# Kernel tuning notes

Hardware: AMD Instinct MI355X
Metric: run time of the kernel (lower is better)

## Reference

```python
import jax, jax.numpy as jnp
import numpy as np

T, D_IN, D_OUT, E, K = 4096, 1024, 1024, 8, 2
H = max(D_IN, D_OUT) * 4  # 4096, per nbHidden = max(nbIn, nbOut) * 4


def setup_inputs() -> dict:
    key = jax.random.key(0)
    ks = jax.random.split(key, 12)
    s = 0.02
    return {
        "x": jax.random.normal(ks[0], (T, D_IN), dtype=jnp.float32),
        "noise": jax.random.normal(ks[1], (T, E), dtype=jnp.float32),
        "gate_w": jax.random.normal(ks[2], (D_IN, E), dtype=jnp.float32) * s,
        "gate_b": jnp.zeros((E,), dtype=jnp.float32),
        "noise_w": jax.random.normal(ks[3], (D_IN, E), dtype=jnp.float32) * s,
        "noise_b": jnp.zeros((E,), dtype=jnp.float32),
        "w1": jax.random.normal(ks[4], (E, D_IN, H), dtype=jnp.float32) * s,
        "b1": jnp.zeros((E, H), dtype=jnp.float32),
        "w2": jax.random.normal(ks[5], (E, H, D_OUT), dtype=jnp.float32) * s,
        "b2": jnp.zeros((E, D_OUT), dtype=jnp.float32),
    }


def reference(x, noise, gate_w, gate_b, noise_w, noise_b, w1, b1, w2, b2):
    # Noisy gating: gate(x) + randn * softplus(noise(x))
    logits = (x @ gate_w + gate_b) + noise * jax.nn.softplus(x @ noise_w + noise_b)  # [T, E]
    topk_vals, topk_idx = jax.lax.top_k(logits, K)          # [T, K]
    gate_prob = jax.nn.softmax(topk_vals, axis=1)           # softmax over selected K logits
    rows = jnp.arange(x.shape[0])[:, None]
    weights = jnp.zeros((x.shape[0], E), dtype=x.dtype).at[rows, topk_idx].set(gate_prob)  # [T, E]

    # Dense path (memMode=False): run every expert MLP on all tokens, masked combine.
    h = jax.nn.relu(jnp.einsum("ti,eih->teh", x, w1) + b1[None])   # [T, E, H]
    expert_out = jnp.einsum("teh,eho->teo", h, w2) + b2[None]       # [T, E, O]
    x_out = jnp.einsum("te,teo->to", weights, expert_out)           # [T, O]
    return x_out, weights
```

## Files before the change

### kernel.cpp

```cpp
#include <hip/hip_runtime.h>

#define T_TOK 4096
#define DIN   1024
#define DOUT  1024
#define NEXP  8
#define HDIM  4096
#define RCAP  9216
#define MT128 80

typedef float f32x4 __attribute__((ext_vector_type(4)));
typedef short bf16x8 __attribute__((ext_vector_type(8)));
typedef unsigned short u16x4 __attribute__((ext_vector_type(4)));
typedef unsigned short u16x8 __attribute__((ext_vector_type(8)));

__device__ __forceinline__ float bf2f(unsigned short u) {
    union { unsigned int i; float f; } v; v.i = ((unsigned int)u) << 16; return v.f;
}
__device__ __forceinline__ unsigned short f2bf(float f) {
    union { unsigned int i; float f; } v; v.f = f;
    unsigned int r = v.i + 0x7FFFu + ((v.i >> 16) & 1u);
    return (unsigned short)(r >> 16);
}

__global__ __launch_bounds__(64) void gating_kernel(
    const float* __restrict__ x, const float* __restrict__ noise,
    const float* __restrict__ gw, const float* __restrict__ gb,
    const float* __restrict__ nw, const float* __restrict__ nb,
    float* __restrict__ wout,
    int* __restrict__ tok_e, float* __restrict__ tok_p)
{
    int t = blockIdx.x;
    int lane = threadIdx.x;
    const float* xr = x + (size_t)t * DIN;
    double ag[NEXP], an[NEXP];
#pragma unroll
    for (int e = 0; e < NEXP; ++e) { ag[e] = 0.0; an[e] = 0.0; }
    for (int d = lane; d < DIN; d += 64) {
        double xv = (double)xr[d];
        const f32x4* g4 = (const f32x4*)(gw + (size_t)d * NEXP);
        const f32x4* n4 = (const f32x4*)(nw + (size_t)d * NEXP);
        f32x4 ga = g4[0], gbv = g4[1], na = n4[0], nbv = n4[1];
#pragma unroll
        for (int j = 0; j < 4; ++j) {
            ag[j]     += xv * (double)ga[j];
            ag[4 + j] += xv * (double)gbv[j];
            an[j]     += xv * (double)na[j];
            an[4 + j] += xv * (double)nbv[j];
        }
    }
#pragma unroll
    for (int e = 0; e < NEXP; ++e) {
        double g = ag[e], n = an[e];
#pragma unroll
        for (int m = 32; m > 0; m >>= 1) { g += __shfl_xor(g, m); n += __shfl_xor(n, m); }
        ag[e] = g; an[e] = n;
    }
    double lg[NEXP];
#pragma unroll
    for (int e = 0; e < NEXP; ++e) {
        double z = an[e] + (double)nb[e];
        double sp = fmax(z, 0.0) + log1p(exp(-fabs(z)));
        lg[e] = ag[e] + (double)gb[e] + (double)noise[(size_t)t * NEXP + e] * sp;
    }
    int i0 = 0; double v0 = lg[0];
#pragma unroll
    for (int e = 1; e < NEXP; ++e) if (lg[e] > v0) { v0 = lg[e]; i0 = e; }
    int i1 = -1; double v1 = -1.0e300;
#pragma unroll
    for (int e = 0; e < NEXP; ++e) if (e != i0 && lg[e] > v1) { v1 = lg[e]; i1 = e; }
    double d1 = exp(v1 - v0);
    float p0 = (float)(1.0 / (1.0 + d1));
    float p1 = (float)(d1 / (1.0 + d1));
    if (lane < NEXP) {
        float wv = (lane == i0) ? p0 : ((lane == i1) ? p1 : 0.0f);
        wout[(size_t)t * NEXP + lane] = wv;
    }
    if (lane == 0) {
        tok_e[2 * t] = i0;     tok_e[2 * t + 1] = i1;
        tok_p[2 * t] = p0;     tok_p[2 * t + 1] = p1;
    }
}

__global__ __launch_bounds__(256) void scan_kernel(
    const int* __restrict__ tok_e, int* __restrict__ tok_slot, int* __restrict__ cnt)
{
    __shared__ int wsum[4];
    int e = blockIdx.x;
    int tid = threadIdx.x;
    int wv = tid >> 6;
    int lane = tid & 63;
    int base = 0;
    for (int c = 0; c < 2 * T_TOK; c += 256) {
        int i = c + tid;
        int m = (tok_e[i] == e) ? 1 : 0;
        unsigned long long bal = __ballot(m);
        int before = __popcll(bal & ((1ull << lane) - 1ull));
        if (lane == 0) wsum[wv] = __popcll(bal);
        __syncthreads();
        int woff = 0;
#pragma unroll
        for (int w = 0; w < 4; ++w) if (w < wv) woff += wsum[w];
        if (m) tok_slot[i] = base + woff + before;
        int tot = wsum[0] + wsum[1] + wsum[2] + wsum[3];
        __syncthreads();
        base += tot;
    }
    if (tid == 0) cnt[e] = base;
}

__global__ void prefix_kernel(const int* __restrict__ cnt, int* __restrict__ poff,
                              int* __restrict__ t2e, int* __restrict__ trow)
{
    if (threadIdx.x != 0 || blockIdx.x != 0) return;
    int base = 0, a = 0;
    for (int e = 0; e < NEXP; ++e) {
        poff[e] = base;
        int c = cnt[e];
        int nt = (c + 127) >> 7;
        for (int i = 0; i < nt; ++i) { t2e[a] = e; trow[a] = base + (i << 7); ++a; }
        base += nt << 7;
    }
    for (; a < MT128; ++a) { t2e[a] = -1; trow[a] = 0; }
}

__global__ __launch_bounds__(256) void gather_kernel(
    const float* __restrict__ x, const int* __restrict__ tok_e,
    const int* __restrict__ tok_slot, const int* __restrict__ poff,
    unsigned short* __restrict__ Xg)
{
    int b = blockIdx.x;
    int t = b >> 1, k = b & 1;
    int e = tok_e[2 * t + k];
    int row = poff[e] + tok_slot[2 * t + k];
    int c = threadIdx.x << 2;
    f32x4 v = *(const f32x4*)(x + (size_t)t * DIN + c);
    u16x4 o;
#pragma unroll
    for (int j = 0; j < 4; ++j) o[j] = f2bf(v[j]);
    *(u16x4*)(Xg + (size_t)row * DIN + c) = o;
}

__global__ __launch_bounds__(256) void convw_kernel(
    const float* __restrict__ W, unsigned short* __restrict__ Wt, int K, int N)
{
    __shared__ float tile[64][65];
    int e = blockIdx.x;
    int k0 = blockIdx.y << 6;
    int n0 = blockIdx.z << 6;
    int tid = threadIdx.x;
    const float* src = W + ((size_t)e * K + k0) * N + n0;
    int r = tid >> 4, c4 = (tid & 15) << 2;
#pragma unroll
    for (int i = 0; i < 4; ++i) {
        f32x4 v = *(const f32x4*)(src + (size_t)(r + (i << 4)) * N + c4);
        *(f32x4*)(&tile[r + (i << 4)][c4]) = v;
    }
    __syncthreads();
    unsigned short* dst = Wt + ((size_t)e * N + n0) * K + k0;
#pragma unroll
    for (int i = 0; i < 2; ++i) {
        int u = (i << 8) + tid;
        int n = u >> 3, kk = (u & 7) << 3;
        u16x8 o;
#pragma unroll
        for (int q = 0; q < 8; ++q) o[q] = f2bf(tile[kk + q][n]);
        *(u16x8*)(dst + (size_t)n * K + kk) = o;
    }
}

__global__ __launch_bounds__(256, 4) void gemm64_kernel(
    const unsigned short* __restrict__ A, int lda,
    const unsigned short* __restrict__ Bt, int ldb, int N, int KLEN,
    unsigned short* __restrict__ C,
    const float* __restrict__ bias,
    const int* __restrict__ t2e, const int* __restrict__ trow,
    int nbshift, int relu)
{
    int nwg = gridDim.x;
    int cpx = nwg >> 3;
    int wg = ((blockIdx.x & 7) * cpx) + (blockIdx.x >> 3);
    int tileid = wg >> nbshift;
    int nb = wg & ((1 << nbshift) - 1);

    int e = t2e[tileid];
    if (e < 0) return;
    int row0 = trow[tileid];
    int n0 = nb << 7;

    __shared__ __align__(16) unsigned short As[128 * 64];
    __shared__ __align__(16) unsigned short Bs[128 * 64];

    int tid = threadIdx.x;
    int lane = tid & 63;
    int wv = tid >> 6;
    int wr = (wv >> 1) << 6;
    int wc = (wv & 1) << 6;

    const unsigned short* Ab = A + (size_t)row0 * lda;
    const unsigned short* Bb = Bt + ((size_t)e * N + n0) * ldb;

    f32x4 acc[4][4] = {};

    int sr_lo = tid >> 3;
    int sp = tid & 7;
    int hr = lane & 15;
    int q4 = lane >> 4;

    int nkt = KLEN >> 6;
    for (int kt = 0; kt < nkt; ++kt) {
        __syncthreads();
        int kb = kt << 6;
#pragma unroll
        for (int i = 0; i < 4; ++i) {
            int r = (i << 5) + sr_lo;
            int col = ((sp ^ (r & 7)) << 3);
            int u = (i << 8) + tid;
            __builtin_amdgcn_global_load_lds(
                (const __attribute__((address_space(1))) void*)(Ab + (size_t)r * lda + kb + col),
                (__attribute__((address_space(3))) void*)(&As[u << 3]), 16, 0, 0);
            __builtin_amdgcn_global_load_lds(
                (const __attribute__((address_space(1))) void*)(Bb + (size_t)r * ldb + kb + col),
                (__attribute__((address_space(3))) void*)(&Bs[u << 3]), 16, 0, 0);
        }
        __syncthreads();
#pragma unroll
        for (int kq = 0; kq < 2; ++kq) {
            int slog = (kq << 2) | q4;
            bf16x8 af[4], bfv[4];
#pragma unroll
            for (int m = 0; m < 4; ++m) {
                int r = wr + (m << 4) + hr;
                af[m] = *(const bf16x8*)(&As[(r << 6) + ((slog ^ (r & 7)) << 3)]);
            }
#pragma unroll
            for (int n = 0; n < 4; ++n) {
                int r = wc + (n << 4) + hr;
                bfv[n] = *(const bf16x8*)(&Bs[(r << 6) + ((slog ^ (r & 7)) << 3)]);
            }
#pragma unroll
            for (int m = 0; m < 4; ++m)
#pragma unroll
                for (int n = 0; n < 4; ++n)
                    acc[m][n] = __builtin_amdgcn_mfma_f32_16x16x32_bf16(af[m], bfv[n], acc[m][n], 0, 0, 0);
        }
    }

    int rq = q4 << 2;
    int cl = hr;
#pragma unroll
    for (int n = 0; n < 4; ++n) {
        int col = wc + (n << 4) + cl;
        float bv = bias[(size_t)e * N + n0 + col];
#pragma unroll
        for (int m = 0; m < 4; ++m) {
#pragma unroll
            for (int r = 0; r < 4; ++r) {
                int row = wr + (m << 4) + rq + r;
                float v = acc[m][n][r] + bv;
                if (relu) v = fmaxf(v, 0.0f);
                C[(size_t)(row0 + row) * N + n0 + col] = f2bf(v);
            }
        }
    }
}

__global__ __launch_bounds__(256) void combine_kernel(
    const unsigned short* __restrict__ O, const int* __restrict__ tok_e,
    const int* __restrict__ tok_slot, const float* __restrict__ tok_p,
    const int* __restrict__ poff, float* __restrict__ xout)
{
    int t = blockIdx.x;
    int e0 = tok_e[2 * t], e1 = tok_e[2 * t + 1];
    int r0 = poff[e0] + tok_slot[2 * t];
    int r1 = poff[e1] + tok_slot[2 * t + 1];
    float p0 = tok_p[2 * t], p1 = tok_p[2 * t + 1];
    int c = threadIdx.x << 2;
    u16x4 a = *(const u16x4*)(O + (size_t)r0 * DOUT + c);
    u16x4 b = *(const u16x4*)(O + (size_t)r1 * DOUT + c);
    f32x4 r;
#pragma unroll
    for (int j = 0; j < 4; ++j) r[j] = p0 * bf2f(a[j]) + p1 * bf2f(b[j]);
    *(f32x4*)(xout + (size_t)t * DOUT + c) = r;
}

extern "C" void kernel_launch(void* const* d_in, const int* in_sizes, int n_in,
                              void* d_out, int out_size, void* d_ws, size_t ws_size,
                              hipStream_t stream)
{
    const float* x     = (const float*)d_in[0];
    const float* noise = (const float*)d_in[1];
    const float* gw    = (const float*)d_in[2];
    const float* gb    = (const float*)d_in[3];
    const float* nw    = (const float*)d_in[4];
    const float* nb    = (const float*)d_in[5];
    const float* w1    = (const float*)d_in[6];
    const float* b1    = (const float*)d_in[7];
    const float* w2    = (const float*)d_in[8];
    const float* b2    = (const float*)d_in[9];
    float* xout = (float*)d_out;
    float* wout = xout + (size_t)T_TOK * DOUT;

    char* ws = (char*)d_ws;
    int*   cnt      = (int*)(ws + 0);
    int*   poff     = (int*)(ws + 256);
    int*   t2e      = (int*)(ws + 512);
    int*   trow     = (int*)(ws + 1024);
    int*   tok_e    = (int*)(ws + 2048);
    int*   tok_slot = (int*)(ws + 34816);
    float* tok_p    = (float*)(ws + 67584);
    size_t oXg = 104448;
    unsigned short* Xg  = (unsigned short*)(ws + oXg);
    unsigned short* O   = Xg;
    size_t oH  = oXg + (size_t)RCAP * DIN * 2;
    unsigned short* H   = (unsigned short*)(ws + oH);
    size_t oW1 = oH + (size_t)RCAP * HDIM * 2;
    unsigned short* W1t = (unsigned short*)(ws + oW1);
    size_t oW2 = oW1 + (size_t)NEXP * HDIM * DIN * 2;
    unsigned short* W2t = (unsigned short*)(ws + oW2);

    gating_kernel<<<T_TOK, 64, 0, stream>>>(x, noise, gw, gb, nw, nb,
                                            wout, tok_e, tok_p);
    scan_kernel<<<NEXP, 256, 0, stream>>>(tok_e, tok_slot, cnt);
    prefix_kernel<<<1, 1, 0, stream>>>(cnt, poff, t2e, trow);
    gather_kernel<<<2 * T_TOK, 256, 0, stream>>>(x, tok_e, tok_slot, poff, Xg);
    convw_kernel<<<dim3(NEXP, DIN / 64, HDIM / 64), 256, 0, stream>>>(w1, W1t, DIN, HDIM);
    convw_kernel<<<dim3(NEXP, HDIM / 64, DOUT / 64), 256, 0, stream>>>(w2, W2t, HDIM, DOUT);
    gemm64_kernel<<<MT128 * 32, 256, 0, stream>>>(
        Xg, DIN, W1t, DIN, HDIM, DIN, H, b1, t2e, trow, 5, 1);
    gemm64_kernel<<<MT128 * 8, 256, 0, stream>>>(
        H, HDIM, W2t, HDIM, DOUT, HDIM, O, b2, t2e, trow, 3, 0);
    combine_kernel<<<T_TOK, 256, 0, stream>>>(O, tok_e, tok_slot, tok_p, poff, xout);
}
```

Before: 356.7 us.

## Double-buffer LDS tiles in expert GEMM to overlap loads with MFMA

Replaces the single LDS tile pair with two ping-pong buffers so the global-to-LDS load of the next K tile is issued while the MFMA work on the current tile runs. This removes the load-then-wait stall at every K step and one barrier per iteration. In exchange, LDS use doubles to 64KB per block and the launch bound drops from 4 to 2 blocks per CU, which reduces occupancy and the latency hiding that came from running more blocks at once. The loop assumes an even number of K tiles.

```diff
diff --git a/kernel.cpp b/kernel.cpp
--- a/kernel.cpp
+++ b/kernel.cpp
@@ -168,7 +168,7 @@
     }
 }
 
-__global__ __launch_bounds__(256, 4) void gemm64_kernel(
+__global__ __launch_bounds__(256, 2) void gemm64_kernel(
     const unsigned short* __restrict__ A, int lda,
     const unsigned short* __restrict__ Bt, int ldb, int N, int KLEN,
     unsigned short* __restrict__ C,
@@ -187,8 +187,10 @@
     int row0 = trow[tileid];
     int n0 = nb << 7;
 
-    __shared__ __align__(16) unsigned short As[128 * 64];
-    __shared__ __align__(16) unsigned short Bs[128 * 64];
+    __shared__ __align__(16) unsigned short As0[128 * 64];
+    __shared__ __align__(16) unsigned short Bs0[128 * 64];
+    __shared__ __align__(16) unsigned short As1[128 * 64];
+    __shared__ __align__(16) unsigned short Bs1[128 * 64];
 
     int tid = threadIdx.x;
     int lane = tid & 63;
@@ -206,44 +208,60 @@
     int hr = lane & 15;
     int q4 = lane >> 4;
 
+#define STAGE(AS, BS, KT)                                                              \
+    {                                                                                  \
+        int kb = (KT) << 6;                                                            \
+        _Pragma("unroll")                                                              \
+        for (int i = 0; i < 4; ++i) {                                                  \
+            int r = (i << 5) + sr_lo;                                                  \
+            int col = ((sp ^ (r & 7)) << 3);                                           \
+            int u = (i << 8) + tid;                                                    \
+            __builtin_amdgcn_global_load_lds(                                          \
+                (const __attribute__((address_space(1))) void*)(Ab + (size_t)r * lda + kb + col), \
+                (__attribute__((address_space(3))) void*)(&AS[u << 3]), 16, 0, 0);     \
+            __builtin_amdgcn_global_load_lds(                                          \
+                (const __attribute__((address_space(1))) void*)(Bb + (size_t)r * ldb + kb + col), \
+                (__attribute__((address_space(3))) void*)(&BS[u << 3]), 16, 0, 0);     \
+        }                                                                              \
+    }
+
+#define COMPUTE(AS, BS)                                                                \
+    {                                                                                  \
+        _Pragma("unroll")                                                              \
+        for (int kq = 0; kq < 2; ++kq) {                                               \
+            int slog = (kq << 2) | q4;                                                 \
+            bf16x8 af[4], bfv[4];                                                      \
+            _Pragma("unroll")                                                          \
+            for (int m = 0; m < 4; ++m) {                                              \
+                int r = wr + (m << 4) + hr;                                            \
+                af[m] = *(const bf16x8*)(&AS[(r << 6) + ((slog ^ (r & 7)) << 3)]);     \
+            }                                                                          \
+            _Pragma("unroll")                                                          \
+            for (int n = 0; n < 4; ++n) {                                              \
+                int r = wc + (n << 4) + hr;                                            \
+                bfv[n] = *(const bf16x8*)(&BS[(r << 6) + ((slog ^ (r & 7)) << 3)]);    \
+            }                                                                          \
+            _Pragma("unroll")                                                          \
+            for (int m = 0; m < 4; ++m)                                                \
+                _Pragma("unroll")                                                      \
+                for (int n = 0; n < 4; ++n)                                            \
+                    acc[m][n] = __builtin_amdgcn_mfma_f32_16x16x32_bf16(af[m], bfv[n], acc[m][n], 0, 0, 0); \
+        }                                                                              \
+    }
+
     int nkt = KLEN >> 6;
-    for (int kt = 0; kt < nkt; ++kt) {
+    STAGE(As0, Bs0, 0);
+    __syncthreads();
+    for (int kt = 0; kt < nkt; kt += 2) {
+        STAGE(As1, Bs1, kt + 1);
+        COMPUTE(As0, Bs0);
         __syncthreads();
-        int kb = kt << 6;
-#pragma unroll
-        for (int i = 0; i < 4; ++i) {
-            int r = (i << 5) + sr_lo;
-            int col = ((sp ^ (r & 7)) << 3);
-            int u = (i << 8) + tid;
-            __builtin_amdgcn_global_load_lds(
-                (const __attribute__((address_space(1))) void*)(Ab + (size_t)r * lda + kb + col),
-                (__attribute__((address_space(3))) void*)(&As[u << 3]), 16, 0, 0);
-            __builtin_amdgcn_global_load_lds(
-                (const __attribute__((address_space(1))) void*)(Bb + (size_t)r * ldb + kb + col),
-                (__attribute__((address_space(3))) void*)(&Bs[u << 3]), 16, 0, 0);
-        }
+        if (kt + 2 < nkt) STAGE(As0, Bs0, kt + 2);
+        COMPUTE(As1, Bs1);
         __syncthreads();
-#pragma unroll
-        for (int kq = 0; kq < 2; ++kq) {
-            int slog = (kq << 2) | q4;
-            bf16x8 af[4], bfv[4];
-#pragma unroll
-            for (int m = 0; m < 4; ++m) {
-                int r = wr + (m << 4) + hr;
-                af[m] = *(const bf16x8*)(&As[(r << 6) + ((slog ^ (r & 7)) << 3)]);
-            }
-#pragma unroll
-            for (int n = 0; n < 4; ++n) {
-                int r = wc + (n << 4) + hr;
-                bfv[n] = *(const bf16x8*)(&Bs[(r << 6) + ((slog ^ (r & 7)) << 3)]);
-            }
-#pragma unroll
-            for (int m = 0; m < 4; ++m)
-#pragma unroll
-                for (int n = 0; n < 4; ++n)
-                    acc[m][n] = __builtin_amdgcn_mfma_f32_16x16x32_bf16(af[m], bfv[n], acc[m][n], 0, 0, 0);
-        }
-    }
+    }
+#undef STAGE
+#undef COMPUTE
 
     int rq = q4 << 2;
     int cl = hr;
```

Measured after the change: 390.5 us. 1.09x slower.

## Use 128x256 tile 512-thread kernel for first expert GEMM and merge weight conversions

Applied to the files above, without the earlier changes.

Replaces the first expert GEMM with a dedicated kernel using 512 threads and a 128x256 output tile, where each wave computes a 64x64 sub-tile from swizzled LDS filled by direct global-to-LDS loads. This raises arithmetic intensity per loaded tile and halves the number of workgroups. The two weight transpose/convert launches are also merged into one kernel to save a launch. The larger tile uses more LDS and registers per block, which may reduce occupancy, and the GEMM loop remains single-buffered.

```diff
diff --git a/kernel.cpp b/kernel.cpp
--- a/kernel.cpp
+++ b/kernel.cpp
@@ -140,13 +140,22 @@
     *(u16x4*)(Xg + (size_t)row * DIN + c) = o;
 }
 
-__global__ __launch_bounds__(256) void convw_kernel(
-    const float* __restrict__ W, unsigned short* __restrict__ Wt, int K, int N)
+__global__ __launch_bounds__(256) void convw2x_kernel(
+    const float* __restrict__ w1, unsigned short* __restrict__ W1t,
+    const float* __restrict__ w2, unsigned short* __restrict__ W2t)
 {
     __shared__ float tile[64][65];
     int e = blockIdx.x;
-    int k0 = blockIdx.y << 6;
-    int n0 = blockIdx.z << 6;
+    int idx = blockIdx.y;
+    const float* W; unsigned short* Wt; int K, N, k0, n0;
+    if (idx < 1024) {
+        W = w1; Wt = W1t; K = DIN; N = HDIM;
+        k0 = (idx >> 6) << 6; n0 = (idx & 63) << 6;
+    } else {
+        int i2 = idx - 1024;
+        W = w2; Wt = W2t; K = HDIM; N = DOUT;
+        k0 = (i2 >> 4) << 6; n0 = (i2 & 15) << 6;
+    }
     int tid = threadIdx.x;
     const float* src = W + ((size_t)e * K + k0) * N + n0;
     int r = tid >> 4, c4 = (tid & 15) << 2;
@@ -165,6 +174,102 @@
 #pragma unroll
         for (int q = 0; q < 8; ++q) o[q] = f2bf(tile[kk + q][n]);
         *(u16x8*)(dst + (size_t)n * K + kk) = o;
+    }
+}
+
+__global__ __launch_bounds__(512, 4) void gemm1_wide_kernel(
+    const unsigned short* __restrict__ A,
+    const unsigned short* __restrict__ Bt,
+    unsigned short* __restrict__ C,
+    const float* __restrict__ bias,
+    const int* __restrict__ t2e, const int* __restrict__ trow)
+{
+    const int lda = DIN, ldb = DIN, N = HDIM;
+    int cpx = gridDim.x >> 3;
+    int wg = ((blockIdx.x & 7) * cpx) + (blockIdx.x >> 3);
+    int tileid = wg >> 4;
+    int nb = wg & 15;
+    int e = t2e[tileid];
+    if (e < 0) return;
+    int row0 = trow[tileid];
+    int n0 = nb << 8;
+
+    __shared__ __align__(16) unsigned short As[128 * 64];
+    __shared__ __align__(16) unsigned short Bs[256 * 64];
+
+    int tid = threadIdx.x;
+    int lane = tid & 63;
+    int wv = tid >> 6;
+    int wr = (wv >> 2) << 6;
+    int wc = (wv & 3) << 6;
+
+    const unsigned short* Ab = A + (size_t)row0 * lda;
+    const unsigned short* Bb = Bt + ((size_t)e * N + n0) * ldb;
+
+    f32x4 acc[4][4] = {};
+    int hr = lane & 15;
+    int q4 = lane >> 4;
+
+    for (int kt = 0; kt < 16; ++kt) {
+        __syncthreads();
+        int kb = kt << 6;
+#pragma unroll
+        for (int i = 0; i < 2; ++i) {
+            int u = (i << 9) + tid;
+            int r = u >> 3, sp = u & 7;
+            int col = ((sp ^ (r & 7)) << 3);
+            __builtin_amdgcn_global_load_lds(
+                (const __attribute__((address_space(1))) void*)(Ab + (size_t)r * lda + kb + col),
+                (__attribute__((address_space(3))) void*)(&As[u << 3]), 16, 0, 0);
+        }
+#pragma unroll
+        for (int i = 0; i < 4; ++i) {
+            int u = (i << 9) + tid;
+            int r = u >> 3, sp = u & 7;
+            int col = ((sp ^ (r & 7)) << 3);
+            __builtin_amdgcn_global_load_lds(
+                (const __attribute__((address_space(1))) void*)(Bb + (size_t)r * ldb + kb + col),
+                (__attribute__((address_space(3))) void*)(&Bs[u << 3]), 16, 0, 0);
+        }
+        __syncthreads();
+#pragma unroll
+        for (int kq = 0; kq < 2; ++kq) {
+            int slog = (kq << 2) | q4;
+            bf16x8 af[4], bfv[4];
+#pragma unroll
+            for (int m = 0; m < 4; ++m) {
+                int r = wr + (m << 4) + hr;
+                af[m] = *(const bf16x8*)(&As[(r << 6) + ((slog ^ (r & 7)) << 3)]);
+            }
+#pragma unroll
+            for (int n = 0; n < 4; ++n) {
+                int r = wc + (n << 4) + hr;
+                bfv[n] = *(const bf16x8*)(&Bs[(r << 6) + ((slog ^ (r & 7)) << 3)]);
+            }
+#pragma unroll
+            for (int m = 0; m < 4; ++m)
+#pragma unroll
+                for (int n = 0; n < 4; ++n)
+                    acc[m][n] = __builtin_amdgcn_mfma_f32_16x16x32_bf16(af[m], bfv[n], acc[m][n], 0, 0, 0);
+        }
+    }
+
+    int rq = q4 << 2;
+    int cl = hr;
+#pragma unroll
+    for (int n = 0; n < 4; ++n) {
+        int col = wc + (n << 4) + cl;
+        float bv = bias[(size_t)e * N + n0 + col];
+#pragma unroll
+        for (int m = 0; m < 4; ++m) {
+#pragma unroll
+            for (int r = 0; r < 4; ++r) {
+                int row = wr + (m << 4) + rq + r;
+                float v = acc[m][n][r] + bv;
+                v = fmaxf(v, 0.0f);
+                C[(size_t)(row0 + row) * N + n0 + col] = f2bf(v);
+            }
+        }
     }
 }
 
@@ -323,10 +428,9 @@
     scan_kernel<<<NEXP, 256, 0, stream>>>(tok_e, tok_slot, cnt);
     prefix_kernel<<<1, 1, 0, stream>>>(cnt, poff, t2e, trow);
     gather_kernel<<<2 * T_TOK, 256, 0, stream>>>(x, tok_e, tok_slot, poff, Xg);
-    convw_kernel<<<dim3(NEXP, DIN / 64, HDIM / 64), 256, 0, stream>>>(w1, W1t, DIN, HDIM);
-    convw_kernel<<<dim3(NEXP, HDIM / 64, DOUT / 64), 256, 0, stream>>>(w2, W2t, HDIM, DOUT);
-    gemm64_kernel<<<MT128 * 32, 256, 0, stream>>>(
-        Xg, DIN, W1t, DIN, HDIM, DIN, H, b1, t2e, trow, 5, 1);
+    convw2x_kernel<<<dim3(NEXP, 2048), 256, 0, stream>>>(w1, W1t, w2, W2t);
+    gemm1_wide_kernel<<<MT128 * 16, 512, 0, stream>>>(
+        Xg, W1t, H, b1, t2e, trow);
     gemm64_kernel<<<MT128 * 8, 256, 0, stream>>>(
         H, HDIM, W2t, HDIM, DOUT, HDIM, O, b2, t2e, trow, 3, 0);
     combine_kernel<<<T_TOK, 256, 0, stream>>>(O, tok_e, tok_slot, tok_p, poff, xout);
```

Measured after the change: 335.1 us. 1.06x faster.
